# Performance work log

Measured on AMD Instinct MI355X. Metric: run time of the kernel, lower is better.

Reference implementation:

```python
import jax, jax.numpy as jnp
import numpy as np

NHID = 1024
NHEAD = 16
HEAD_DIM = 64
B, L = 8, 4096

def setup_inputs() -> dict:
    key = jax.random.key(0)
    ks = jax.random.split(key, 12)
    s_in = 1.0 / np.sqrt(NHID)
    s_o = 1.0 / np.sqrt(NHEAD * HEAD_DIM)
    return {
        'x': jax.random.normal(ks[0], (B, L, NHID), dtype=jnp.float32),
        'ax': jax.random.normal(ks[1], (B, NHID), dtype=jnp.float32),
        'WQ_w': jax.random.normal(ks[2], (NHID, NHEAD * HEAD_DIM), dtype=jnp.float32) * s_in,
        'WQ_b': jnp.zeros((NHEAD * HEAD_DIM,), dtype=jnp.float32),
        'WK_w': jax.random.normal(ks[3], (NHID, NHEAD * HEAD_DIM), dtype=jnp.float32) * s_in,
        'WK_b': jnp.zeros((NHEAD * HEAD_DIM,), dtype=jnp.float32),
        'WV_w': jax.random.normal(ks[4], (NHID, NHEAD * HEAD_DIM), dtype=jnp.float32) * s_in,
        'WV_b': jnp.zeros((NHEAD * HEAD_DIM,), dtype=jnp.float32),
        'WO_w': jax.random.normal(ks[5], (NHEAD * HEAD_DIM, NHID), dtype=jnp.float32) * s_o,
        'WO_b': jnp.zeros((NHID,), dtype=jnp.float32),
    }

def reference(x, ax, WQ_w, WQ_b, WK_w, WK_b, WV_w, WV_b, WO_w, WO_b):
    Bx, Lx, H = x.shape
    nh, d = NHEAD, HEAD_DIM
    q = (x @ WQ_w + WQ_b).reshape(Bx, Lx, nh, d)
    k = (x @ WK_w + WK_b).reshape(Bx, Lx, nh, d)
    # global token projections (note: source's v local slots use K due to pad_v=F.pad(k,...) bug)
    ak = (ax @ WK_w + WK_b).reshape(Bx, 1, nh, d)
    av = (ax @ WV_w + WV_b).reshape(Bx, 1, nh, d)
    # shifted local window (unfold_size=3), pad seq dim by 1 on each side
    pad_k = jnp.pad(k, ((0, 0), (1, 1), (0, 0), (0, 0)))  # (B, L+2, nh, d)
    k_shift = jnp.stack([pad_k[:, t:Lx + t] for t in range(3)], axis=3)  # (B,L,nh,3,d)
    akb = jnp.broadcast_to(ak, (Bx, Lx, nh, d))[:, :, :, None, :]  # (B,L,nh,1,d)
    avb = jnp.broadcast_to(av, (Bx, Lx, nh, d))[:, :, :, None, :]
    K = jnp.concatenate([akb, k_shift], axis=3)  # (B,L,nh,4,d)
    V = jnp.concatenate([avb, k_shift], axis=3)  # local V slots = K (faithful to source bug)
    scores = jnp.einsum('blhd,blhjd->blhj', q, K) / jnp.sqrt(jnp.float32(d))
    alphas = jax.nn.softmax(scores, axis=-1)  # dropout = identity (eval)
    att = jnp.einsum('blhj,blhjd->blhd', alphas, V).reshape(Bx, Lx, nh * d)
    return att @ WO_w + WO_b
```

## Files before the change

### kernel.cpp

```cpp
#include <hip/hip_runtime.h>
#include <hip/hip_bf16.h>

typedef __bf16 bf16x8 __attribute__((ext_vector_type(8)));
typedef __bf16 bf16x4 __attribute__((ext_vector_type(4)));
typedef float  floatx4 __attribute__((ext_vector_type(4)));

#define L_SEQ 4096

__global__ void cvt_bf16_kernel(const float* __restrict__ src,
                                __bf16* __restrict__ dst, int n8)
{
    int i = blockIdx.x * blockDim.x + threadIdx.x;
    if (i >= n8) return;
    const float4* s = (const float4*)src + (size_t)i * 2;
    float4 f0 = s[0], f1 = s[1];
    bf16x8 o;
    o[0] = (__bf16)f0.x; o[1] = (__bf16)f0.y; o[2] = (__bf16)f0.z; o[3] = (__bf16)f0.w;
    o[4] = (__bf16)f1.x; o[5] = (__bf16)f1.y; o[6] = (__bf16)f1.z; o[7] = (__bf16)f1.w;
    *((bf16x8*)dst + i) = o;
}

__global__ void transpose_cvt3_kernel(const float* __restrict__ WQ,
                                      const float* __restrict__ WK,
                                      const float* __restrict__ WO,
                                      __bf16* __restrict__ Wqk,
                                      __bf16* __restrict__ Wo)
{
    const int z = blockIdx.z;
    const float* src = (z == 0) ? WQ : (z == 1) ? WK : WO;
    __bf16* dst = (z == 0) ? Wqk : (z == 1) ? (Wqk + (size_t)1024 * 1024) : Wo;

    __shared__ float tile[32][33];
    int tx = threadIdx.x & 31, ty = threadIdx.x >> 5;
    int n0 = blockIdx.x * 32, k0 = blockIdx.y * 32;
    #pragma unroll
    for (int i = 0; i < 32; i += 8)
        tile[ty + i][tx] = src[(size_t)(k0 + ty + i) * 1024 + n0 + tx];
    __syncthreads();
    #pragma unroll
    for (int i = 0; i < 32; i += 8)
        dst[(size_t)(n0 + ty + i) * 1024 + k0 + tx] = (__bf16)tile[tx][ty + i];
}

__global__ void akv_part_kernel(const float* __restrict__ ax,
                                const float* __restrict__ Wk,
                                const float* __restrict__ Wv,
                                float* __restrict__ part)
{
    int b = blockIdx.x, kv = blockIdx.y, z = blockIdx.z;
    int n = threadIdx.x * 4;
    const float* W   = kv ? Wv : Wk;
    const float* axr = ax + (size_t)b * 1024 + z * 128;
    float4 acc = {0.f, 0.f, 0.f, 0.f};
    for (int k = 0; k < 128; ++k) {
        float a = axr[k];
        float4 w = *(const float4*)(W + (size_t)(z * 128 + k) * 1024 + n);
        acc.x = fmaf(a, w.x, acc.x);
        acc.y = fmaf(a, w.y, acc.y);
        acc.z = fmaf(a, w.z, acc.z);
        acc.w = fmaf(a, w.w, acc.w);
    }
    *(float4*)(part + (((size_t)(b * 2 + kv)) * 8 + z) * 1024 + n) = acc;
}

__global__ void akv_reduce_kernel(const float* __restrict__ part,
                                  const float* __restrict__ bk,
                                  const float* __restrict__ bv,
                                  float* __restrict__ akv)
{
    int b = blockIdx.x, kv = blockIdx.y;
    int n = threadIdx.x * 4;
    float4 acc = *(const float4*)((kv ? bv : bk) + n);
    #pragma unroll
    for (int z = 0; z < 8; ++z) {
        float4 p = *(const float4*)(part + (((size_t)(b * 2 + kv)) * 8 + z) * 1024 + n);
        acc.x += p.x; acc.y += p.y; acc.z += p.z; acc.w += p.w;
    }
    *(float4*)(akv + ((size_t)b * 2 + kv) * 1024 + n) = acc;
}

#define GLDS(gp, lp) __builtin_amdgcn_global_load_lds(                              \
    (const __attribute__((address_space(1))) void*)(gp),                            \
    (__attribute__((address_space(3))) void*)(lp), 16, 0, 0)

#define STAGE_A(hi, kt, buf) do {                                                   \
    GLDS(A + aS[0][hi] + (size_t)(kt) * 64, smem + (buf) * 65536 + aD[0][hi]);      \
    GLDS(A + aS[1][hi] + (size_t)(kt) * 64, smem + (buf) * 65536 + aD[1][hi]);      \
} while (0)
#define STAGE_B(hi, kt, buf) do {                                                   \
    GLDS(Bt + bS[0][hi] + (size_t)(kt) * 64, smem + (buf) * 65536 + bD[0][hi]);     \
    GLDS(Bt + bS[1][hi] + (size_t)(kt) * 64, smem + (buf) * 65536 + bD[1][hi]);     \
} while (0)

#define RDA(cb, mi, kk) (*(const bf16x8*)(smem + (cb) + awoff + ((mi) << 11) + ((kk) << 10)))
#define RDB(cb, ni, kk) (*(const bf16x8*)(smem + (cb) + bwoff + ((ni) << 11) + ((kk) << 10)))
#define MFMA16(af, bfv, c) (c) = __builtin_amdgcn_mfma_f32_16x16x32_bf16((af), (bfv), (c), 0, 0, 0)

#define WAIT_LGKM0() do { asm volatile("s_waitcnt lgkmcnt(0)");                     \
    __builtin_amdgcn_sched_barrier(0); } while (0)
#define WAIT_VM(n) do { asm volatile("s_waitcnt vmcnt(" #n ")");                    \
    __builtin_amdgcn_sched_barrier(0); } while (0)
#define SBAR() do { __builtin_amdgcn_sched_barrier(0);                              \
    asm volatile("s_barrier" ::: "memory");                                         \
    __builtin_amdgcn_sched_barrier(0); } while (0)

template <int NT, bool OUT_F32>
__global__ __launch_bounds__(512, 2) void gemm256_kernel(
    const __bf16* __restrict__ A, const __bf16* __restrict__ Bt,
    const float* __restrict__ b0, const float* __restrict__ b1, int nsplit,
    void* __restrict__ Cp, int M, int N, int K)
{
    __shared__ __align__(16) char smem[131072];

    const int bid = blockIdx.x;
    const int xcd = bid & 7, g = bid >> 3;
    const int s = g & 31, r = g >> 5;
    int mt, nt;
    if constexpr (NT == 8) {
        nt = ((xcd & 1) << 2) | (s & 3);
        mt = (r << 5) + ((xcd >> 1) << 3) + (s >> 2);
    } else {
        nt = s & 3;
        mt = (xcd << 4) + (r << 3) + (s >> 2);
    }
    const int m0 = mt << 8, n0 = nt << 8;

    const int tid  = threadIdx.x;
    const int wave = tid >> 6, lane = tid & 63;
    const int l15  = lane & 15, quad = lane >> 4;
    const int ntile = K >> 6;

    const int rowin = lane >> 2;
    const int colel = ((lane & 3) << 3) ^ (((lane >> 5) & 1) << 4);
    size_t aS[2][2], bS[2][2];
    int    aD[2][2], bD[2][2];
    #pragma unroll
    for (int hi = 0; hi < 2; ++hi) {
        const int rgA = (wave & 3) + ((wave >> 2) << 3) + hi * 4;
        const int rgB = ((wave >> 1) << 2) + (wave & 1) + hi * 2;
        #pragma unroll
        for (int c = 0; c < 2; ++c) {
            aS[c][hi] = (size_t)(m0 + rgA * 16 + rowin) * K + c * 32 + colel;
            aD[c][hi] = (rgA * 2 + c) << 10;
            bS[c][hi] = (size_t)(n0 + rgB * 16 + rowin) * K + c * 32 + colel;
            bD[c][hi] = 32768 + ((rgB * 2 + c) << 10);
        }
    }

    const int alane = (l15 << 6) + ((quad << 4) ^ (((l15 >> 3) & 1) << 5));
    const int awoff = (((wave >> 2) * 8) << 11) + alane;
    const int bwoff = 32768 + (((wave & 3) * 4) << 11) + alane;

    floatx4 acc[8][4] = {};

    STAGE_A(0, 0, 0); STAGE_A(1, 0, 0); STAGE_B(0, 0, 0); STAGE_B(1, 0, 0);
    STAGE_A(0, 1, 1); STAGE_B(0, 1, 1); STAGE_B(1, 1, 1);
    WAIT_VM(6);
    SBAR();

    for (int t = 0; t < ntile; ++t) {
        const int p  = t & 1;
        const int cb = p * 65536;
        bf16x8 a0[4][2], a1[4][2], b0f[2][2], b1f[2][2];

        #pragma unroll
        for (int mi = 0; mi < 4; ++mi) { a0[mi][0] = RDA(cb, mi, 0); a0[mi][1] = RDA(cb, mi, 1); }
        #pragma unroll
        for (int ni = 0; ni < 2; ++ni) { b0f[ni][0] = RDB(cb, ni, 0); b0f[ni][1] = RDB(cb, ni, 1); }
        if (t + 1 < ntile) STAGE_A(1, t + 1, p ^ 1);
        SBAR();
        WAIT_LGKM0();
        __builtin_amdgcn_s_setprio(1);
        #pragma unroll
        for (int mi = 0; mi < 4; ++mi)
            #pragma unroll
            for (int ni = 0; ni < 2; ++ni) {
                MFMA16(a0[mi][0], b0f[ni][0], acc[mi][ni]);
                MFMA16(a0[mi][1], b0f[ni][1], acc[mi][ni]);
            }
        __builtin_amdgcn_s_setprio(0);
        SBAR();

        #pragma unroll
        for (int ni = 0; ni < 2; ++ni) { b1f[ni][0] = RDB(cb, ni + 2, 0); b1f[ni][1] = RDB(cb, ni + 2, 1); }
        if (t + 2 < ntile) STAGE_A(0, t + 2, p);
        SBAR();
        WAIT_LGKM0();
        __builtin_amdgcn_s_setprio(1);
        #pragma unroll
        for (int mi = 0; mi < 4; ++mi)
            #pragma unroll
            for (int ni = 0; ni < 2; ++ni) {
                MFMA16(a0[mi][0], b1f[ni][0], acc[mi][ni + 2]);
                MFMA16(a0[mi][1], b1f[ni][1], acc[mi][ni + 2]);
            }
        __builtin_amdgcn_s_setprio(0);
        SBAR();

        #pragma unroll
        for (int mi = 0; mi < 4; ++mi) { a1[mi][0] = RDA(cb, mi + 4, 0); a1[mi][1] = RDA(cb, mi + 4, 1); }
        if (t + 2 < ntile) STAGE_B(0, t + 2, p);
        SBAR();
        WAIT_LGKM0();
        __builtin_amdgcn_s_setprio(1);
        #pragma unroll
        for (int mi = 0; mi < 4; ++mi)
            #pragma unroll
            for (int ni = 0; ni < 2; ++ni) {
                MFMA16(a1[mi][0], b1f[ni][0], acc[mi + 4][ni + 2]);
                MFMA16(a1[mi][1], b1f[ni][1], acc[mi + 4][ni + 2]);
            }
        __builtin_amdgcn_s_setprio(0);
        SBAR();

        if (t + 2 < ntile) {
            STAGE_B(1, t + 2, p);
            WAIT_VM(6);
        } else {
            WAIT_VM(0);
        }
        SBAR();
        __builtin_amdgcn_s_setprio(1);
        #pragma unroll
        for (int mi = 0; mi < 4; ++mi)
            #pragma unroll
            for (int ni = 0; ni < 2; ++ni) {
                MFMA16(a1[mi][0], b0f[ni][0], acc[mi + 4][ni]);
                MFMA16(a1[mi][1], b0f[ni][1], acc[mi + 4][ni]);
            }
        __builtin_amdgcn_s_setprio(0);
        SBAR();
    }

    const int gmw = m0 + (wave >> 2) * 128;
    const int gnw = n0 + (wave & 3) * 64;
    #pragma unroll
    for (int ni = 0; ni < 4; ++ni) {
        int gn = gnw + ni * 16 + l15;
        float bv = (gn < nsplit) ? b0[gn] : b1[gn - nsplit];
        #pragma unroll
        for (int mi = 0; mi < 8; ++mi) {
            int gm = gmw + mi * 16 + quad * 4;
            #pragma unroll
            for (int r = 0; r < 4; ++r) {
                float v = acc[mi][ni][r] + bv;
                if constexpr (OUT_F32)
                    ((float*)Cp)[(size_t)(gm + r) * N + gn] = v;
                else
                    ((__bf16*)Cp)[(size_t)(gm + r) * N + gn] = (__bf16)v;
            }
        }
    }
}

__global__ void attn_kernel(const __bf16* __restrict__ qk,
                            const float* __restrict__ akv,
                            __bf16* __restrict__ att)
{
    const int t  = threadIdx.x;
    const int c4 = t * 4;
    const int m0 = blockIdx.x * 8;
    const int l0 = m0 & (L_SEQ - 1);
    const int b  = m0 >> 12;

    float kr[10][4];
    #pragma unroll
    for (int j = 0; j < 10; ++j) {
        int ll = l0 - 1 + j;
        if (ll >= 0 && ll < L_SEQ) {
            bf16x4 kv = *(const bf16x4*)(qk + (size_t)(m0 - 1 + j) * 2048 + 1024 + c4);
            kr[j][0] = kv[0]; kr[j][1] = kv[1]; kr[j][2] = kv[2]; kr[j][3] = kv[3];
        } else {
            kr[j][0] = kr[j][1] = kr[j][2] = kr[j][3] = 0.f;
        }
    }
    float4 ak4 = *(const float4*)(akv + ((size_t)b * 2 + 0) * 1024 + c4);
    float4 av4 = *(const float4*)(akv + ((size_t)b * 2 + 1) * 1024 + c4);

    #pragma unroll
    for (int i = 0; i < 8; ++i) {
        const int m = m0 + i;
        bf16x4 qv = *(const bf16x4*)(qk + (size_t)m * 2048 + c4);
        float q0 = qv[0], q1 = qv[1], q2 = qv[2], q3 = qv[3];

        float p0 = q0 * ak4.x + q1 * ak4.y + q2 * ak4.z + q3 * ak4.w;
        float p1 = q0 * kr[i][0]     + q1 * kr[i][1]     + q2 * kr[i][2]     + q3 * kr[i][3];
        float p2 = q0 * kr[i + 1][0] + q1 * kr[i + 1][1] + q2 * kr[i + 1][2] + q3 * kr[i + 1][3];
        float p3 = q0 * kr[i + 2][0] + q1 * kr[i + 2][1] + q2 * kr[i + 2][2] + q3 * kr[i + 2][3];
        #pragma unroll
        for (int off = 1; off < 16; off <<= 1) {
            p0 += __shfl_xor(p0, off, 64);
            p1 += __shfl_xor(p1, off, 64);
            p2 += __shfl_xor(p2, off, 64);
            p3 += __shfl_xor(p3, off, 64);
        }
        const float sc = 0.125f;
        float s0 = p0 * sc, s1 = p1 * sc, s2 = p2 * sc, s3 = p3 * sc;
        float mx = fmaxf(fmaxf(s0, s1), fmaxf(s2, s3));
        float e0 = __expf(s0 - mx), e1 = __expf(s1 - mx), e2 = __expf(s2 - mx), e3 = __expf(s3 - mx);
        float inv = 1.f / (e0 + e1 + e2 + e3);

        bf16x4 o;
        o[0] = (__bf16)((e0 * av4.x + e1 * kr[i][0] + e2 * kr[i + 1][0] + e3 * kr[i + 2][0]) * inv);
        o[1] = (__bf16)((e0 * av4.y + e1 * kr[i][1] + e2 * kr[i + 1][1] + e3 * kr[i + 2][1]) * inv);
        o[2] = (__bf16)((e0 * av4.z + e1 * kr[i][2] + e2 * kr[i + 1][2] + e3 * kr[i + 2][2]) * inv);
        o[3] = (__bf16)((e0 * av4.w + e1 * kr[i][3] + e2 * kr[i + 1][3] + e3 * kr[i + 2][3]) * inv);
        *(bf16x4*)(att + (size_t)m * 1024 + c4) = o;
    }
}

extern "C" void kernel_launch(void* const* d_in, const int* in_sizes, int n_in,
                              void* d_out, int out_size, void* d_ws, size_t ws_size,
                              hipStream_t stream)
{
    const float* x    = (const float*)d_in[0];
    const float* ax   = (const float*)d_in[1];
    const float* WQ_w = (const float*)d_in[2];
    const float* WQ_b = (const float*)d_in[3];
    const float* WK_w = (const float*)d_in[4];
    const float* WK_b = (const float*)d_in[5];
    const float* WV_w = (const float*)d_in[6];
    const float* WV_b = (const float*)d_in[7];
    const float* WO_w = (const float*)d_in[8];
    const float* WO_b = (const float*)d_in[9];
    float* out = (float*)d_out;

    const int M = 8 * 4096;

    char* ws = (char*)d_ws;
    __bf16* xb   = (__bf16*)(ws);
    __bf16* Wqk  = (__bf16*)(ws + 67108864);
    __bf16* Wo   = (__bf16*)(ws + 71303168);
    __bf16* qk   = (__bf16*)(ws + 73400320);
    __bf16* att  = (__bf16*)(ws + 207618048);
    float*  akv  = (float*)(ws + 274726912);
    float*  akvp = (float*)(ws + 274792448);

    {
        int n8 = (M * 1024) / 8;
        cvt_bf16_kernel<<<n8 / 256, 256, 0, stream>>>(x, xb, n8);
    }
    transpose_cvt3_kernel<<<dim3(32, 32, 3), 256, 0, stream>>>(WQ_w, WK_w, WO_w, Wqk, Wo);
    akv_part_kernel<<<dim3(8, 2, 8), 256, 0, stream>>>(ax, WK_w, WV_w, akvp);
    akv_reduce_kernel<<<dim3(8, 2), 256, 0, stream>>>(akvp, WK_b, WV_b, akv);
    gemm256_kernel<8, false><<<(M / 256) * 8, 512, 0, stream>>>(
        xb, Wqk, WQ_b, WK_b, 1024, (void*)qk, M, 2048, 1024);
    attn_kernel<<<M / 8, 256, 0, stream>>>(qk, akv, att);
    gemm256_kernel<4, true><<<(M / 256) * 4, 512, 0, stream>>>(
        att, Wo, WO_b, WO_b, 1024, (void*)out, M, 1024, 1024);
}
```

Before: 544.4 us.

## Remap attention kernel to one thread per head-row, removing shuffle reductions

```diff
diff --git a/kernel.cpp b/kernel.cpp
--- a/kernel.cpp
+++ b/kernel.cpp
@@ -253,59 +253,65 @@
     }
 }
 
-__global__ void attn_kernel(const __bf16* __restrict__ qk,
-                            const float* __restrict__ akv,
-                            __bf16* __restrict__ att)
-{
-    const int t  = threadIdx.x;
-    const int c4 = t * 4;
-    const int m0 = blockIdx.x * 8;
-    const int l0 = m0 & (L_SEQ - 1);
-    const int b  = m0 >> 12;
-
-    float kr[10][4];
-    #pragma unroll
-    for (int j = 0; j < 10; ++j) {
-        int ll = l0 - 1 + j;
-        if (ll >= 0 && ll < L_SEQ) {
-            bf16x4 kv = *(const bf16x4*)(qk + (size_t)(m0 - 1 + j) * 2048 + 1024 + c4);
-            kr[j][0] = kv[0]; kr[j][1] = kv[1]; kr[j][2] = kv[2]; kr[j][3] = kv[3];
-        } else {
-            kr[j][0] = kr[j][1] = kr[j][2] = kr[j][3] = 0.f;
+__global__ __launch_bounds__(256) void attn_kernel(const __bf16* __restrict__ qk,
+                                                   const float* __restrict__ akv,
+                                                   __bf16* __restrict__ att)
+{
+    const int t = threadIdx.x;
+    const int h = t >> 4;
+    const int i = t & 15;
+    const int m = blockIdx.x * 16 + i;
+    const int l = m & (L_SEQ - 1);
+    const int b = m >> 12;
+
+    const __bf16* qrow = qk + (size_t)m * 2048 + h * 64;
+    const __bf16* krow = qk + (size_t)m * 2048 + 1024 + h * 64;
+    const float*  akr  = akv + ((size_t)b * 2 + 0) * 1024 + h * 64;
+    const float*  avr  = akv + ((size_t)b * 2 + 1) * 1024 + h * 64;
+    const bool vm = (l >= 1), vp = (l <= L_SEQ - 2);
+
+    float sA = 0.f, s0 = 0.f, s1 = 0.f, s2 = 0.f;
+    #pragma unroll
+    for (int c = 0; c < 8; ++c) {
+        bf16x8 qc = *(const bf16x8*)(qrow + c * 8);
+        bf16x8 k1 = *(const bf16x8*)(krow + c * 8);
+        bf16x8 k0 = {}, k2 = {};
+        if (vm) k0 = *(const bf16x8*)(krow - 2048 + c * 8);
+        if (vp) k2 = *(const bf16x8*)(krow + 2048 + c * 8);
+        float a[8];
+        *(float4*)(a)     = *(const float4*)(akr + c * 8);
+        *(float4*)(a + 4) = *(const float4*)(akr + c * 8 + 4);
+        #pragma unroll
+        for (int d = 0; d < 8; ++d) {
+            float qd = (float)qc[d];
+            sA = fmaf(qd, a[d], sA);
+            s0 = fmaf(qd, (float)k0[d], s0);
+            s1 = fmaf(qd, (float)k1[d], s1);
+            s2 = fmaf(qd, (float)k2[d], s2);
         }
     }
-    float4 ak4 = *(const float4*)(akv + ((size_t)b * 2 + 0) * 1024 + c4);
-    float4 av4 = *(const float4*)(akv + ((size_t)b * 2 + 1) * 1024 + c4);
-
-    #pragma unroll
-    for (int i = 0; i < 8; ++i) {
-        const int m = m0 + i;
-        bf16x4 qv = *(const bf16x4*)(qk + (size_t)m * 2048 + c4);
-        float q0 = qv[0], q1 = qv[1], q2 = qv[2], q3 = qv[3];
-
-        float p0 = q0 * ak4.x + q1 * ak4.y + q2 * ak4.z + q3 * ak4.w;
-        float p1 = q0 * kr[i][0]     + q1 * kr[i][1]     + q2 * kr[i][2]     + q3 * kr[i][3];
-        float p2 = q0 * kr[i + 1][0] + q1 * kr[i + 1][1] + q2 * kr[i + 1][2] + q3 * kr[i + 1][3];
-        float p3 = q0 * kr[i + 2][0] + q1 * kr[i + 2][1] + q2 * kr[i + 2][2] + q3 * kr[i + 2][3];
-        #pragma unroll
-        for (int off = 1; off < 16; off <<= 1) {
-            p0 += __shfl_xor(p0, off, 64);
-            p1 += __shfl_xor(p1, off, 64);
-            p2 += __shfl_xor(p2, off, 64);
-            p3 += __shfl_xor(p3, off, 64);
-        }
-        const float sc = 0.125f;
-        float s0 = p0 * sc, s1 = p1 * sc, s2 = p2 * sc, s3 = p3 * sc;
-        float mx = fmaxf(fmaxf(s0, s1), fmaxf(s2, s3));
-        float e0 = __expf(s0 - mx), e1 = __expf(s1 - mx), e2 = __expf(s2 - mx), e3 = __expf(s3 - mx);
-        float inv = 1.f / (e0 + e1 + e2 + e3);
-
-        bf16x4 o;
-        o[0] = (__bf16)((e0 * av4.x + e1 * kr[i][0] + e2 * kr[i + 1][0] + e3 * kr[i + 2][0]) * inv);
-        o[1] = (__bf16)((e0 * av4.y + e1 * kr[i][1] + e2 * kr[i + 1][1] + e3 * kr[i + 2][1]) * inv);
-        o[2] = (__bf16)((e0 * av4.z + e1 * kr[i][2] + e2 * kr[i + 1][2] + e3 * kr[i + 2][2]) * inv);
-        o[3] = (__bf16)((e0 * av4.w + e1 * kr[i][3] + e2 * kr[i + 1][3] + e3 * kr[i + 2][3]) * inv);
-        *(bf16x4*)(att + (size_t)m * 1024 + c4) = o;
+    const float sc = 0.125f;
+    sA *= sc; s0 *= sc; s1 *= sc; s2 *= sc;
+    float mx = fmaxf(fmaxf(sA, s0), fmaxf(s1, s2));
+    float eA = __expf(sA - mx), e0 = __expf(s0 - mx), e1 = __expf(s1 - mx), e2 = __expf(s2 - mx);
+    float inv = 1.f / (eA + e0 + e1 + e2);
+    eA *= inv; e0 *= inv; e1 *= inv; e2 *= inv;
+
+    __bf16* orow = att + (size_t)m * 1024 + h * 64;
+    #pragma unroll
+    for (int c = 0; c < 8; ++c) {
+        bf16x8 k1 = *(const bf16x8*)(krow + c * 8);
+        bf16x8 k0 = {}, k2 = {};
+        if (vm) k0 = *(const bf16x8*)(krow - 2048 + c * 8);
+        if (vp) k2 = *(const bf16x8*)(krow + 2048 + c * 8);
+        float a[8];
+        *(float4*)(a)     = *(const float4*)(avr + c * 8);
+        *(float4*)(a + 4) = *(const float4*)(avr + c * 8 + 4);
+        bf16x8 o;
+        #pragma unroll
+        for (int d = 0; d < 8; ++d)
+            o[d] = (__bf16)(eA * a[d] + e0 * (float)k0[d] + e1 * (float)k1[d] + e2 * (float)k2[d]);
+        *(bf16x8*)(orow + c * 8) = o;
     }
 }
 
@@ -345,7 +351,7 @@
     akv_reduce_kernel<<<dim3(8, 2), 256, 0, stream>>>(akvp, WK_b, WV_b, akv);
     gemm256_kernel<8, false><<<(M / 256) * 8, 512, 0, stream>>>(
         xb, Wqk, WQ_b, WK_b, 1024, (void*)qk, M, 2048, 1024);
-    attn_kernel<<<M / 8, 256, 0, stream>>>(qk, akv, att);
+    attn_kernel<<<M / 16, 256, 0, stream>>>(qk, akv, att);
     gemm256_kernel<4, true><<<(M / 256) * 4, 512, 0, stream>>>(
         att, Wo, WO_b, WO_b, 1024, (void*)out, M, 1024, 1024);
 }
```

Result: slower. 678.8 us (+24.7%).
